# Kernel optimization log

Hardware: AMD Instinct MI355X
Metric: run time of the kernel (lower is better)

## Reference

```python
import math
import jax, jax.numpy as jnp
import numpy as np

SCORE_THR = 0.05
NMS_THR = 0.5
MIN_SIZE = 0.01
MAX_DET = 100
SCALE_CLAMP = math.log(1000.0 / 16.0)
WX, WY, WW, WH = 10.0, 10.0, 5.0, 5.0  # BoxCoder weights


def setup_inputs() -> dict:
    key = jax.random.key(0)
    k1, k2, k3, k4 = jax.random.split(key, 4)
    B, N, C = 4, 2048, 3
    H = W = 800
    class_logits = 2.0 * jax.random.normal(k1, (B, N, C), dtype=jnp.float32)
    box_regression = 0.5 * jax.random.normal(k2, (B, N, 4 * C), dtype=jnp.float32)
    cxy = jax.random.uniform(k3, (B, N, 2), minval=0.0, maxval=float(W))
    wh = jax.random.uniform(k4, (B, N, 2), minval=4.0, maxval=100.0)
    proposals = jnp.concatenate([cxy - 0.5 * wh, cxy + 0.5 * wh], axis=-1)
    proposals = jnp.clip(proposals, 0.0, float(W))
    return {"class_logits": class_logits, "box_regression": box_regression,
            "proposals": proposals, "image_h": H, "image_w": W}


def _decode(rel, props):
    # rel: [N, C, 4] deltas, props: [N, 4] xyxy -> [N, C, 4] decoded boxes
    w = props[:, 2] - props[:, 0]
    h = props[:, 3] - props[:, 1]
    cx = props[:, 0] + 0.5 * w
    cy = props[:, 1] + 0.5 * h
    dx = rel[..., 0] / WX
    dy = rel[..., 1] / WY
    dw = jnp.minimum(rel[..., 2] / WW, SCALE_CLAMP)
    dh = jnp.minimum(rel[..., 3] / WH, SCALE_CLAMP)
    pcx = dx * w[:, None] + cx[:, None]
    pcy = dy * h[:, None] + cy[:, None]
    pw = jnp.exp(dw) * w[:, None]
    ph = jnp.exp(dh) * h[:, None]
    return jnp.stack([pcx - 0.5 * pw, pcy - 0.5 * ph,
                      pcx + 0.5 * pw, pcy + 0.5 * ph], axis=-1)


def _pairwise_iou(b):
    # b: [M, 4] -> [M, M]
    area = (b[:, 2] - b[:, 0]) * (b[:, 3] - b[:, 1])
    lt = jnp.maximum(b[:, None, :2], b[None, :, :2])
    rb = jnp.minimum(b[:, None, 2:], b[None, :, 2:])
    whd = jnp.clip(rb - lt, 0.0)
    inter = whd[..., 0] * whd[..., 1]
    return inter / (area[:, None] + area[None, :] - inter + 1e-7)


def _per_image(logits, rel, props, H, W):
    N, C = logits.shape
    scores = jax.nn.softmax(logits, axis=-1)               # [N, C]
    boxes = _decode(rel.reshape(N, C, 4), props)           # [N, C, 4]
    # clip to image (x in [0,W], y in [0,H])
    boxes = jnp.stack([jnp.clip(boxes[..., 0], 0.0, W),
                       jnp.clip(boxes[..., 1], 0.0, H),
                       jnp.clip(boxes[..., 2], 0.0, W),
                       jnp.clip(boxes[..., 3], 0.0, H)], axis=-1)
    # drop background class and flatten -> M = N*(C-1)
    boxes = boxes[:, 1:, :].reshape(-1, 4)
    scores = scores[:, 1:].reshape(-1)
    labels = jnp.broadcast_to(jnp.arange(1, C), (N, C - 1)).reshape(-1)
    valid = ((scores > SCORE_THR)
             & (boxes[:, 2] - boxes[:, 0] >= MIN_SIZE)
             & (boxes[:, 3] - boxes[:, 1] >= MIN_SIZE))
    # batched_nms via per-class coordinate offset
    offset = labels.astype(boxes.dtype) * (jnp.max(boxes) + 1.0)
    ob = boxes + offset[:, None]
    sort_key = jnp.where(valid, scores, -jnp.inf)
    order = jnp.argsort(-sort_key)
    bs, ss, ls, vs, obs = boxes[order], scores[order], labels[order], valid[order], ob[order]
    iou = _pairwise_iou(obs)                               # [M, M]
    M = bs.shape[0]
    idxs = jnp.arange(M)
    def body(i, keep):
        sup = keep[i] & (iou[i] > NMS_THR) & (idxs > i)
        return keep & ~sup
    keep = jax.lax.fori_loop(0, M, body, vs)
    sel = jnp.argsort(~keep, stable=True)[:MAX_DET]        # kept first, score order preserved
    kb, ksc, kl, kk = bs[sel], ss[sel], ls[sel], keep[sel]
    kb = jnp.where(kk[:, None], kb, 0.0)
    ksc = jnp.where(kk, ksc, 0.0)
    kl = jnp.where(kk, kl, 0)
    return kb, ksc, kl, kk


def reference(class_logits, box_regression, proposals, image_h, image_w):
    H = jnp.float32(image_h)
    W = jnp.float32(image_w)
    f = jax.vmap(lambda l, r, p: _per_image(l, r, p, H, W))
    boxes, scores, labels, keep = f(class_logits, box_regression, proposals)
    return boxes, scores, labels, keep
```

## Files before the change

### kernel.cpp

```cpp
#include <hip/hip_runtime.h>
#include <stdint.h>

#define BB 4
#define NN 2048
#define CC 3
#define MM (NN * (CC - 1))
#define MAXDET 100
#define SCORE_THR 0.05f
#define NMS_THR 0.5f
#define MIN_SIZE 0.01f
#define TTARGET 512
#define SSKCAP 1024

#define SCORE_OFF (BB * MAXDET * 4)
#define LABEL_OFF (SCORE_OFF + BB * MAXDET)
#define KEEP_OFF (LABEL_OFF + BB * MAXDET)
#define STASH(b, j) (SCORE_OFF + (b) * MAXDET + 96 + (j))

__device__ __forceinline__ void wave_lds_sync() {
  __builtin_amdgcn_wave_barrier();
  __builtin_amdgcn_s_waitcnt(0xC07F);
  __builtin_amdgcn_wave_barrier();
}

__global__ __launch_bounds__(512) void decode_kernel(const float* __restrict__ logits,
                                                     const float* __restrict__ rel,
                                                     const float* __restrict__ props,
                                                     const int* __restrict__ ph,
                                                     const int* __restrict__ pw,
                                                     float4* __restrict__ cand_box,
                                                     unsigned long long* __restrict__ keys,
                                                     float* __restrict__ out) {
#pragma clang fp contract(off)
  __shared__ float red[512];
  int tid = threadIdx.x;
  int t = blockIdx.x * 512 + tid;
  int b = t >> 11;
  int n = t & 2047;
  float Hf = (float)ph[0];
  float Wf = (float)pw[0];

  const float* lg = logits + (size_t)t * CC;
  float l0 = lg[0], l1 = lg[1], l2 = lg[2];
  float mx = fmaxf(l0, fmaxf(l1, l2));
  float e0 = expf(l0 - mx), e1 = expf(l1 - mx), e2 = expf(l2 - mx);
  float ssum = (e0 + e1) + e2;

  float4 pr = ((const float4*)props)[t];
  float w = pr.z - pr.x, h = pr.w - pr.y;
  float cx = pr.x + 0.5f * w, cy = pr.y + 0.5f * h;
  const float4* rl = (const float4*)(rel + (size_t)t * 12);
  const float SCALE_CLAMP = 4.135166556742356f;

  float lmax = 0.0f;
  for (int c = 1; c < CC; ++c) {
    float4 rv = rl[c];
    float score = (c == 1 ? e1 : e2) / ssum;
    float dx = rv.x / 10.0f;
    float dy = rv.y / 10.0f;
    float dw = fminf(rv.z / 5.0f, SCALE_CLAMP);
    float dh = fminf(rv.w / 5.0f, SCALE_CLAMP);
    float pcx = dx * w + cx;
    float pcy = dy * h + cy;
    float bw = expf(dw) * w;
    float bh = expf(dh) * h;
    float x1 = pcx - 0.5f * bw, y1 = pcy - 0.5f * bh;
    float x2 = pcx + 0.5f * bw, y2 = pcy + 0.5f * bh;
    x1 = fminf(fmaxf(x1, 0.0f), Wf);
    y1 = fminf(fmaxf(y1, 0.0f), Hf);
    x2 = fminf(fmaxf(x2, 0.0f), Wf);
    y2 = fminf(fmaxf(y2, 0.0f), Hf);

    lmax = fmaxf(lmax, fmaxf(fmaxf(x1, y1), fmaxf(x2, y2)));

    bool valid = (score > SCORE_THR) && (x2 - x1 >= MIN_SIZE) && (y2 - y1 >= MIN_SIZE);
    int m = n * (CC - 1) + (c - 1);
    cand_box[(size_t)b * MM + m] = make_float4(x1, y1, x2, y2);
    unsigned long long key = 0ull;
    if (valid)
      key = (((unsigned long long)__float_as_uint(score)) << 32) |
            (unsigned long long)(0xFFFFFFFFu - (unsigned)m);
    keys[(size_t)b * MM + m] = key;
  }

  red[tid] = lmax;
  __syncthreads();
  for (int s2 = 256; s2 > 0; s2 >>= 1) {
    if (tid < s2) red[tid] = fmaxf(red[tid], red[tid + s2]);
    __syncthreads();
  }
  if (tid == 0) out[STASH(b, blockIdx.x & 3)] = red[0];
}

__device__ void bitonic_sort_desc(unsigned long long* a, int P, int tid) {
  int prev_big = 1;
  for (int size = 2; size <= P; size <<= 1) {
    for (int stride = size >> 1; stride > 0; stride >>= 1) {
      int big = (stride >= 128);
      if (big | prev_big) __syncthreads(); else wave_lds_sync();
      for (int i = tid; i < (P >> 1); i += 512) {
        int lo = 2 * i - (i & (stride - 1));
        int hi = lo + stride;
        bool asc = ((lo & size) != 0);
        unsigned long long x = a[lo], y = a[hi];
        if ((x > y) == asc) { a[lo] = y; a[hi] = x; }
      }
      prev_big = big;
    }
  }
  __syncthreads();
}

__device__ __forceinline__ int run_nms(const unsigned long long* skeys, int count,
                                       const float4* sbox, int G,
                                       const float4* __restrict__ cbg, float off_base,
                                       int b, float* __restrict__ out) {
#pragma clang fp contract(off)
  int lane = threadIdx.x;
  float4 kob0 = make_float4(0, 0, 0, 0), kob1 = make_float4(0, 0, 0, 0);
  float4 kraw0 = make_float4(0, 0, 0, 0), kraw1 = make_float4(0, 0, 0, 0);
  float karea0 = 0.0f, karea1 = 0.0f, ksc0 = 0.0f, ksc1 = 0.0f;
  int klb0 = 0, klb1 = 0;
  int cnt = 0;

  unsigned long long key0 = (count > 0) ? skeys[0] : 0ull;
  unsigned long long key1 = (count > 1) ? skeys[1] : 0ull;
  float4 bx0 = make_float4(0, 0, 0, 0);
  if (count > 0) bx0 = sbox[0];

  for (int i = 0; i < count; ++i) {
    unsigned long long key2 = (i + 2 < count) ? skeys[i + 2] : 0ull;
    float4 bx1 = make_float4(0, 0, 0, 0);
    if (i + 1 < count) {
      int m1 = (int)(0xFFFFFFFFu - (unsigned)key1);
      bx1 = (i + 1 < G) ? sbox[i + 1] : cbg[m1];
    }

    unsigned hik = (unsigned)(key0 >> 32);
    if (hik == 0u) break;
    int m = (int)(0xFFFFFFFFu - (unsigned)key0);
    int lbl = (m & 1) + 1;
    float off = (float)lbl * off_base;
    float ax1 = bx0.x + off, ay1 = bx0.y + off;
    float ax2 = bx0.z + off, ay2 = bx0.w + off;
    float aarea = (ax2 - ax1) * (ay2 - ay1);

    bool sup = false;
    if (lane < cnt) {
      float ltx = fmaxf(kob0.x, ax1), lty = fmaxf(kob0.y, ay1);
      float rbx = fminf(kob0.z, ax2), rby = fminf(kob0.w, ay2);
      float iw = fmaxf(rbx - ltx, 0.0f), ih = fmaxf(rby - lty, 0.0f);
      float inter = iw * ih;
      float denom = ((karea0 + aarea) - inter) + 1e-7f;
      if (inter / denom > NMS_THR) sup = true;
    }
    if (lane + 64 < cnt) {
      float ltx = fmaxf(kob1.x, ax1), lty = fmaxf(kob1.y, ay1);
      float rbx = fminf(kob1.z, ax2), rby = fminf(kob1.w, ay2);
      float iw = fmaxf(rbx - ltx, 0.0f), ih = fmaxf(rby - lty, 0.0f);
      float inter = iw * ih;
      float denom = ((karea1 + aarea) - inter) + 1e-7f;
      if (inter / denom > NMS_THR) sup = true;
    }
    if (!__any(sup)) {
      if (cnt < 64) {
        if (lane == cnt) {
          kob0 = make_float4(ax1, ay1, ax2, ay2);
          kraw0 = bx0;
          karea0 = aarea;
          ksc0 = __uint_as_float(hik);
          klb0 = lbl;
        }
      } else {
        if (lane == cnt - 64) {
          kob1 = make_float4(ax1, ay1, ax2, ay2);
          kraw1 = bx0;
          karea1 = aarea;
          ksc1 = __uint_as_float(hik);
          klb1 = lbl;
        }
      }
      cnt++;
      if (cnt >= MAXDET) break;
    }
    key0 = key1;
    key1 = key2;
    bx0 = bx1;
  }

  for (int r = 0; r < 2; ++r) {
    int s = r * 64 + lane;
    if (s < cnt) {
      float4 bx = r ? kraw1 : kraw0;
      float sc = r ? ksc1 : ksc0;
      int lb = r ? klb1 : klb0;
      float* obp = out + (size_t)b * MAXDET * 4 + (size_t)s * 4;
      obp[0] = bx.x; obp[1] = bx.y; obp[2] = bx.z; obp[3] = bx.w;
      out[SCORE_OFF + b * MAXDET + s] = sc;
      out[LABEL_OFF + b * MAXDET + s] = (float)lb;
      out[KEEP_OFF + b * MAXDET + s] = 1.0f;
    }
  }
  return cnt;
}

__global__ __launch_bounds__(512) void nms_kernel(const float4* __restrict__ cand_box,
                                                  const unsigned long long* __restrict__ keys,
                                                  float* __restrict__ out) {
#pragma clang fp contract(off)
  __shared__ __align__(16) unsigned long long sk[MM];
  __shared__ __align__(16) unsigned long long ssk[SSKCAP];
  __shared__ float4 sbox[SSKCAP];
  __shared__ unsigned hist[1024];
  __shared__ int s_scnt, s_thr, s_vtot, s_cnt, s_fb;

  int b = blockIdx.x;
  int tid = threadIdx.x;
  int lane = tid & 63;
  const float4* cbg = cand_box + (size_t)b * MM;

  const ulonglong2* kg = (const ulonglong2*)(keys + (size_t)b * MM);
  ulonglong2 kr[4];
#pragma unroll
  for (int j = 0; j < 4; ++j) kr[j] = kg[j * 512 + tid];

  hist[tid] = 0u;
  hist[tid + 512] = 0u;
  if (tid == 0) { s_scnt = 0; s_thr = 0; s_fb = 0; s_cnt = 0; }
  float m01 = fmaxf(out[STASH(b, 0)], out[STASH(b, 1)]);
  float m23 = fmaxf(out[STASH(b, 2)], out[STASH(b, 3)]);
  float off_base = fmaxf(m01, m23) + 1.0f;
  __syncthreads();

#pragma unroll
  for (int j = 0; j < 4; ++j) {
    unsigned h0 = (unsigned)(kr[j].x >> 32);
    unsigned h1 = (unsigned)(kr[j].y >> 32);
    if (h0) atomicAdd(&hist[(h0 >> 16) & 1023], 1u);
    if (h1) atomicAdd(&hist[(h1 >> 16) & 1023], 1u);
  }
  __syncthreads();

  if (tid < 64) {
    unsigned own[16];
#pragma unroll
    for (int i = 0; i < 16; ++i) own[i] = hist[tid * 16 + i];
    unsigned psum = 0;
#pragma unroll
    for (int i = 0; i < 16; ++i) psum += own[i];
    unsigned s = psum;
    for (int d = 1; d < 64; d <<= 1) {
      unsigned o = __shfl_down(s, d);
      if (tid + d < 64) s += o;
    }
    unsigned after = s - psum;
    int best = -1;
    unsigned run = after;
#pragma unroll
    for (int i = 15; i >= 0; --i) {
      run += own[i];
      if (best < 0 && run >= TTARGET) best = tid * 16 + i;
    }
    int gb = best;
    for (int d = 1; d < 64; d <<= 1) {
      int o = __shfl_down(gb, d);
      if (tid + d < 64) gb = (o > gb) ? o : gb;
    }
    if (tid == 0) {
      s_thr = (gb < 0) ? 0 : gb;
      s_vtot = (int)s;
    }
  }
  __syncthreads();
  int thr = s_thr;
  int Vtot = s_vtot;

#pragma unroll
  for (int j = 0; j < 8; ++j) {
    unsigned long long key = (j & 1) ? kr[j >> 1].y : kr[j >> 1].x;
    unsigned hik = (unsigned)(key >> 32);
    bool pred = (hik != 0u) && ((int)((hik >> 16) & 1023) >= thr);
    unsigned long long mask = __ballot(pred);
    int ofs = __popcll(mask & ((1ull << lane) - 1ull));
    int base = 0;
    if (lane == 0 && mask) base = atomicAdd(&s_scnt, (int)__popcll(mask));
    base = __shfl(base, 0);
    if (pred) {
      int pos = base + ofs;
      if (pos < SSKCAP) ssk[pos] = key;
    }
  }
  __syncthreads();
  int T = s_scnt;

  if (T <= SSKCAP) {
    int P = 1;
    while (P < T) P <<= 1;
    for (int i = T + tid; i < P; i += 512) ssk[i] = 0ull;
    __syncthreads();
    bitonic_sort_desc(ssk, P, tid);
    for (int jj = tid; jj < T; jj += 512) {
      int m = (int)(0xFFFFFFFFu - (unsigned)ssk[jj]);
      sbox[jj] = cbg[m];
    }
    __syncthreads();
    if (tid < 64) {
      int cnt = run_nms(ssk, T, sbox, SSKCAP, cbg, off_base, b, out);
      if (tid == 0) {
        s_cnt = cnt;
        s_fb = (cnt < MAXDET && T < Vtot) ? 1 : 0;
      }
    }
  } else {
    if (tid == 0) s_fb = 1;
  }
  __syncthreads();

  if (s_fb) {
    ulonglong2* skp = (ulonglong2*)sk;
#pragma unroll
    for (int j = 0; j < 4; ++j) skp[j * 512 + tid] = kr[j];
    __syncthreads();
    bitonic_sort_desc(sk, MM, tid);
    int Gf = (Vtot < SSKCAP) ? Vtot : SSKCAP;
    for (int jj = tid; jj < Gf; jj += 512) {
      int m = (int)(0xFFFFFFFFu - (unsigned)sk[jj]);
      sbox[jj] = cbg[m];
    }
    __syncthreads();
    if (tid < 64) {
      int cnt = run_nms(sk, Vtot, sbox, Gf, cbg, off_base, b, out);
      if (tid == 0) s_cnt = cnt;
    }
    __syncthreads();
  }

  int cnt = s_cnt;
  if (tid >= cnt && tid < MAXDET) {
    float* obp = out + (size_t)b * MAXDET * 4 + (size_t)tid * 4;
    obp[0] = 0.0f; obp[1] = 0.0f; obp[2] = 0.0f; obp[3] = 0.0f;
    out[SCORE_OFF + b * MAXDET + tid] = 0.0f;
    out[LABEL_OFF + b * MAXDET + tid] = 0.0f;
    out[KEEP_OFF + b * MAXDET + tid] = 0.0f;
  }
}

extern "C" void kernel_launch(void* const* d_in, const int* in_sizes, int n_in,
                              void* d_out, int out_size, void* d_ws, size_t ws_size,
                              hipStream_t stream) {
  const float* logits = (const float*)d_in[0];
  const float* rel = (const float*)d_in[1];
  const float* props = (const float*)d_in[2];
  const int* ph = (const int*)d_in[3];
  const int* pw = (const int*)d_in[4];
  float* out = (float*)d_out;

  char* ws = (char*)d_ws;
  float4* cand_box = (float4*)ws;
  unsigned long long* keys = (unsigned long long*)(ws + (size_t)BB * MM * 16);

  decode_kernel<<<16, 512, 0, stream>>>(logits, rel, props, ph, pw, cand_box, keys, out);
  nms_kernel<<<BB, 512, 0, stream>>>(cand_box, keys, out);
}
```

Baseline: 111.9 us.

## Replace serial single-wave NMS with tiled block-parallel bitmask NMS

Replaces the one-wave sequential greedy NMS, which handled one candidate per iteration, with a tiled scheme. Each tile of 128 sorted candidates is loaded into LDS. All 8 waves compute the intra-tile IoU suppression bitmasks and the suppression flags against already-kept boxes in parallel, then one wave resolves the tile serially using shuffles of those masks. The aim is to spread IoU work across the whole block and shorten the serial dependency chain. The cost is several block barriers per tile and a second serial scan, and it may compute IoUs for candidates beyond the point where 100 detections are reached.

Result: faster. 101.0 us (-9.8%).

```diff
diff --git a/kernel.cpp b/kernel.cpp
--- a/kernel.cpp
+++ b/kernel.cpp
@@ -11,6 +11,7 @@
 #define MIN_SIZE 0.01f
 #define TTARGET 512
 #define SSKCAP 1024
+#define TILE 128
 
 #define SCORE_OFF (BB * MAXDET * 4)
 #define LABEL_OFF (SCORE_OFF + BB * MAXDET)
@@ -21,6 +22,17 @@
   __builtin_amdgcn_wave_barrier();
   __builtin_amdgcn_s_waitcnt(0xC07F);
   __builtin_amdgcn_wave_barrier();
+}
+
+__device__ __forceinline__ bool iou_gt(const float4 A, const float aA,
+                                       const float4 B, const float aB) {
+#pragma clang fp contract(off)
+  float ltx = fmaxf(A.x, B.x), lty = fmaxf(A.y, B.y);
+  float rbx = fminf(A.z, B.z), rby = fminf(A.w, B.w);
+  float iw = fmaxf(rbx - ltx, 0.0f), ih = fmaxf(rby - lty, 0.0f);
+  float inter = iw * ih;
+  float denom = ((aA + aB) - inter) + 1e-7f;
+  return inter / denom > NMS_THR;
 }
 
 __global__ __launch_bounds__(512) void decode_kernel(const float* __restrict__ logits,
@@ -111,95 +123,103 @@
   __syncthreads();
 }
 
-__device__ __forceinline__ int run_nms(const unsigned long long* skeys, int count,
-                                       const float4* sbox, int G,
-                                       const float4* __restrict__ cbg, float off_base,
-                                       int b, float* __restrict__ out) {
+__device__ int tiled_nms(const unsigned long long* keys_s, int count,
+                         const float4* __restrict__ cbg, float off_base,
+                         float4* tob, float4* trb, float* tarea,
+                         ulonglong2* smask, int* sflag, int* knew,
+                         float4* kept_ob, float4* kept_raw, float* kept_area,
+                         unsigned long long* kept_key, int* s_nnew, int tid) {
 #pragma clang fp contract(off)
-  int lane = threadIdx.x;
-  float4 kob0 = make_float4(0, 0, 0, 0), kob1 = make_float4(0, 0, 0, 0);
-  float4 kraw0 = make_float4(0, 0, 0, 0), kraw1 = make_float4(0, 0, 0, 0);
-  float karea0 = 0.0f, karea1 = 0.0f, ksc0 = 0.0f, ksc1 = 0.0f;
-  int klb0 = 0, klb1 = 0;
+  int wv = tid >> 6, lane = tid & 63;
   int cnt = 0;
-
-  unsigned long long key0 = (count > 0) ? skeys[0] : 0ull;
-  unsigned long long key1 = (count > 1) ? skeys[1] : 0ull;
-  float4 bx0 = make_float4(0, 0, 0, 0);
-  if (count > 0) bx0 = sbox[0];
-
-  for (int i = 0; i < count; ++i) {
-    unsigned long long key2 = (i + 2 < count) ? skeys[i + 2] : 0ull;
-    float4 bx1 = make_float4(0, 0, 0, 0);
-    if (i + 1 < count) {
-      int m1 = (int)(0xFFFFFFFFu - (unsigned)key1);
-      bx1 = (i + 1 < G) ? sbox[i + 1] : cbg[m1];
-    }
-
-    unsigned hik = (unsigned)(key0 >> 32);
-    if (hik == 0u) break;
-    int m = (int)(0xFFFFFFFFu - (unsigned)key0);
-    int lbl = (m & 1) + 1;
-    float off = (float)lbl * off_base;
-    float ax1 = bx0.x + off, ay1 = bx0.y + off;
-    float ax2 = bx0.z + off, ay2 = bx0.w + off;
-    float aarea = (ax2 - ax1) * (ay2 - ay1);
-
-    bool sup = false;
-    if (lane < cnt) {
-      float ltx = fmaxf(kob0.x, ax1), lty = fmaxf(kob0.y, ay1);
-      float rbx = fminf(kob0.z, ax2), rby = fminf(kob0.w, ay2);
-      float iw = fmaxf(rbx - ltx, 0.0f), ih = fmaxf(rby - lty, 0.0f);
-      float inter = iw * ih;
-      float denom = ((karea0 + aarea) - inter) + 1e-7f;
-      if (inter / denom > NMS_THR) sup = true;
-    }
-    if (lane + 64 < cnt) {
-      float ltx = fmaxf(kob1.x, ax1), lty = fmaxf(kob1.y, ay1);
-      float rbx = fminf(kob1.z, ax2), rby = fminf(kob1.w, ay2);
-      float iw = fmaxf(rbx - ltx, 0.0f), ih = fmaxf(rby - lty, 0.0f);
-      float inter = iw * ih;
-      float denom = ((karea1 + aarea) - inter) + 1e-7f;
-      if (inter / denom > NMS_THR) sup = true;
-    }
-    if (!__any(sup)) {
-      if (cnt < 64) {
-        if (lane == cnt) {
-          kob0 = make_float4(ax1, ay1, ax2, ay2);
-          kraw0 = bx0;
-          karea0 = aarea;
-          ksc0 = __uint_as_float(hik);
-          klb0 = lbl;
+  for (int base = 0; base < count && cnt < MAXDET; base += TILE) {
+    int tsz = (count - base < TILE) ? (count - base) : TILE;
+    if (tid < tsz) {
+      unsigned long long key = keys_s[base + tid];
+      int m = (int)(0xFFFFFFFFu - (unsigned)key);
+      float4 bx = cbg[m];
+      int lbl = (m & 1) + 1;
+      float off = (float)lbl * off_base;
+      float4 ob = make_float4(bx.x + off, bx.y + off, bx.z + off, bx.w + off);
+      tob[tid] = ob;
+      trb[tid] = bx;
+      tarea[tid] = (ob.z - ob.x) * (ob.w - ob.y);
+    }
+    __syncthreads();
+
+    float4 bi0 = tob[lane];
+    float ai0 = tarea[lane];
+    float4 bi1 = tob[lane + 64];
+    float ai1 = tarea[lane + 64];
+    float4 kb0 = kept_ob[(lane < cnt) ? lane : 0];
+    float ka0 = kept_area[(lane < cnt) ? lane : 0];
+    float4 kb1 = kept_ob[(lane + 64 < cnt) ? lane + 64 : 0];
+    float ka1 = kept_area[(lane + 64 < cnt) ? lane + 64 : 0];
+
+    for (int j = wv; j < tsz; j += 8) {
+      float4 aj = tob[j];
+      float aaj = tarea[j];
+      unsigned long long w0 = 0ull, w1 = 0ull;
+      if (j < 63) {
+        bool p = (lane > j) && (lane < tsz) && iou_gt(aj, aaj, bi0, ai0);
+        w0 = __ballot(p);
+      }
+      if (j < 127) {
+        int i = lane + 64;
+        bool p = (i > j) && (i < tsz) && iou_gt(aj, aaj, bi1, ai1);
+        w1 = __ballot(p);
+      }
+      bool s = false;
+      if (cnt > 0) {
+        if (lane < cnt && iou_gt(kb0, ka0, aj, aaj)) s = true;
+        if (cnt > 64 && lane + 64 < cnt && iou_gt(kb1, ka1, aj, aaj)) s = true;
+      }
+      int anyk = __any(s);
+      if (lane == 0) {
+        smask[j].x = w0;
+        smask[j].y = w1;
+        sflag[j] = anyk;
+      }
+    }
+    __syncthreads();
+
+    if (tid < 64) {
+      int iA = 2 * lane, iB = 2 * lane + 1;
+      ulonglong2 rA = smask[(iA < tsz) ? iA : 0];
+      ulonglong2 rB = smask[(iB < tsz) ? iB : 0];
+      int fA = sflag[(iA < tsz) ? iA : 0];
+      int fB = sflag[(iB < tsz) ? iB : 0];
+      unsigned long long r0 = 0ull, r1 = 0ull;
+      int c = cnt, nk = 0;
+      for (int j = 0; j < tsz; ++j) {
+        int src = j >> 1;
+        unsigned long long m0 = __shfl((j & 1) ? rB.x : rA.x, src);
+        unsigned long long m1 = __shfl((j & 1) ? rB.y : rA.y, src);
+        int fl = __shfl((j & 1) ? fB : fA, src);
+        bool rem = (j < 64) ? ((r0 >> j) & 1ull) : ((r1 >> (j - 64)) & 1ull);
+        if (!rem && !fl) {
+          if (lane == 0) knew[nk] = j;
+          nk++;
+          c++;
+          r0 |= m0;
+          r1 |= m1;
+          if (c >= MAXDET) break;
         }
-      } else {
-        if (lane == cnt - 64) {
-          kob1 = make_float4(ax1, ay1, ax2, ay2);
-          kraw1 = bx0;
-          karea1 = aarea;
-          ksc1 = __uint_as_float(hik);
-          klb1 = lbl;
-        }
-      }
-      cnt++;
-      if (cnt >= MAXDET) break;
-    }
-    key0 = key1;
-    key1 = key2;
-    bx0 = bx1;
-  }
-
-  for (int r = 0; r < 2; ++r) {
-    int s = r * 64 + lane;
-    if (s < cnt) {
-      float4 bx = r ? kraw1 : kraw0;
-      float sc = r ? ksc1 : ksc0;
-      int lb = r ? klb1 : klb0;
-      float* obp = out + (size_t)b * MAXDET * 4 + (size_t)s * 4;
-      obp[0] = bx.x; obp[1] = bx.y; obp[2] = bx.z; obp[3] = bx.w;
-      out[SCORE_OFF + b * MAXDET + s] = sc;
-      out[LABEL_OFF + b * MAXDET + s] = (float)lb;
-      out[KEEP_OFF + b * MAXDET + s] = 1.0f;
-    }
+      }
+      if (lane == 0) *s_nnew = nk;
+    }
+    __syncthreads();
+
+    int nnew = *s_nnew;
+    if (tid < nnew) {
+      int j = knew[tid];
+      kept_ob[cnt + tid] = tob[j];
+      kept_raw[cnt + tid] = trb[j];
+      kept_area[cnt + tid] = tarea[j];
+      kept_key[cnt + tid] = keys_s[base + j];
+    }
+    cnt += nnew;
+    __syncthreads();
   }
   return cnt;
 }
@@ -210,9 +230,18 @@
 #pragma clang fp contract(off)
   __shared__ __align__(16) unsigned long long sk[MM];
   __shared__ __align__(16) unsigned long long ssk[SSKCAP];
-  __shared__ float4 sbox[SSKCAP];
   __shared__ unsigned hist[1024];
-  __shared__ int s_scnt, s_thr, s_vtot, s_cnt, s_fb;
+  __shared__ __align__(16) float4 tob[TILE];
+  __shared__ __align__(16) float4 trb[TILE];
+  __shared__ float tarea[TILE];
+  __shared__ __align__(16) ulonglong2 smask[TILE];
+  __shared__ int sflag[TILE];
+  __shared__ int knew[TILE];
+  __shared__ float4 kept_ob[MAXDET];
+  __shared__ float4 kept_raw[MAXDET];
+  __shared__ float kept_area[MAXDET];
+  __shared__ unsigned long long kept_key[MAXDET];
+  __shared__ int s_scnt, s_thr, s_vtot, s_cnt, s_fb, s_nnew;
 
   int b = blockIdx.x;
   int tid = threadIdx.x;
@@ -282,11 +311,11 @@
     bool pred = (hik != 0u) && ((int)((hik >> 16) & 1023) >= thr);
     unsigned long long mask = __ballot(pred);
     int ofs = __popcll(mask & ((1ull << lane) - 1ull));
-    int base = 0;
-    if (lane == 0 && mask) base = atomicAdd(&s_scnt, (int)__popcll(mask));
-    base = __shfl(base, 0);
+    int basea = 0;
+    if (lane == 0 && mask) basea = atomicAdd(&s_scnt, (int)__popcll(mask));
+    basea = __shfl(basea, 0);
     if (pred) {
-      int pos = base + ofs;
+      int pos = basea + ofs;
       if (pos < SSKCAP) ssk[pos] = key;
     }
   }
@@ -299,17 +328,11 @@
     for (int i = T + tid; i < P; i += 512) ssk[i] = 0ull;
     __syncthreads();
     bitonic_sort_desc(ssk, P, tid);
-    for (int jj = tid; jj < T; jj += 512) {
-      int m = (int)(0xFFFFFFFFu - (unsigned)ssk[jj]);
-      sbox[jj] = cbg[m];
-    }
-    __syncthreads();
-    if (tid < 64) {
-      int cnt = run_nms(ssk, T, sbox, SSKCAP, cbg, off_base, b, out);
-      if (tid == 0) {
-        s_cnt = cnt;
-        s_fb = (cnt < MAXDET && T < Vtot) ? 1 : 0;
-      }
+    int cnt = tiled_nms(ssk, T, cbg, off_base, tob, trb, tarea, smask, sflag,
+                        knew, kept_ob, kept_raw, kept_area, kept_key, &s_nnew, tid);
+    if (tid == 0) {
+      s_cnt = cnt;
+      s_fb = (cnt < MAXDET && T < Vtot) ? 1 : 0;
     }
   } else {
     if (tid == 0) s_fb = 1;
@@ -322,26 +345,29 @@
     for (int j = 0; j < 4; ++j) skp[j * 512 + tid] = kr[j];
     __syncthreads();
     bitonic_sort_desc(sk, MM, tid);
-    int Gf = (Vtot < SSKCAP) ? Vtot : SSKCAP;
-    for (int jj = tid; jj < Gf; jj += 512) {
-      int m = (int)(0xFFFFFFFFu - (unsigned)sk[jj]);
-      sbox[jj] = cbg[m];
-    }
-    __syncthreads();
-    if (tid < 64) {
-      int cnt = run_nms(sk, Vtot, sbox, Gf, cbg, off_base, b, out);
-      if (tid == 0) s_cnt = cnt;
-    }
+    int cnt = tiled_nms(sk, Vtot, cbg, off_base, tob, trb, tarea, smask, sflag,
+                        knew, kept_ob, kept_raw, kept_area, kept_key, &s_nnew, tid);
+    if (tid == 0) s_cnt = cnt;
     __syncthreads();
   }
 
   int cnt = s_cnt;
-  if (tid >= cnt && tid < MAXDET) {
+  if (tid < MAXDET) {
+    float4 bx = make_float4(0.0f, 0.0f, 0.0f, 0.0f);
+    float sc = 0.0f, lb = 0.0f, kp = 0.0f;
+    if (tid < cnt) {
+      unsigned long long key = kept_key[tid];
+      int m = (int)(0xFFFFFFFFu - (unsigned)key);
+      bx = kept_raw[tid];
+      sc = __uint_as_float((unsigned)(key >> 32));
+      lb = (float)((m & 1) + 1);
+      kp = 1.0f;
+    }
     float* obp = out + (size_t)b * MAXDET * 4 + (size_t)tid * 4;
-    obp[0] = 0.0f; obp[1] = 0.0f; obp[2] = 0.0f; obp[3] = 0.0f;
-    out[SCORE_OFF + b * MAXDET + tid] = 0.0f;
-    out[LABEL_OFF + b * MAXDET + tid] = 0.0f;
-    out[KEEP_OFF + b * MAXDET + tid] = 0.0f;
+    obp[0] = bx.x; obp[1] = bx.y; obp[2] = bx.z; obp[3] = bx.w;
+    out[SCORE_OFF + b * MAXDET + tid] = sc;
+    out[LABEL_OFF + b * MAXDET + tid] = lb;
+    out[KEEP_OFF + b * MAXDET + tid] = kp;
   }
 }
 
```
